# Optimization experiments

Hardware: AMD Instinct MI355X
Metric: run time of the kernel (lower is better)

Reference implementation:

```python
import jax, jax.numpy as jnp
import numpy as np

DEPTH = 12  # perfect binary tree: 2**DEPTH - 1 internal nodes, 2**DEPTH leaf children


def setup_inputs() -> dict:
    key = jax.random.key(0)
    k0, k1, k2, k3, k4 = jax.random.split(key, 5)
    H = 1024   # hidden_size
    I = 1024   # input_size
    N = 2 ** DEPTH - 1  # internal nodes, heap order (root = 0)
    scale = 0.02  # keep gates out of saturation
    emb = jax.random.normal(k0, (N, I), jnp.float32)
    W_ih = jax.random.normal(k1, (8 * H, I), jnp.float32) * scale
    W_hh = jax.random.normal(k2, (8 * H, 2 * H), jnp.float32) * scale
    b_ih = jax.random.normal(k3, (8 * H,), jnp.float32) * scale
    b_hh = jax.random.normal(k4, (8 * H,), jnp.float32) * scale
    return {"emb": emb, "W_ih": W_ih, "W_hh": W_hh, "b_ih": b_ih, "b_hh": b_hh}


def reference(emb, W_ih, W_hh, b_ih, b_hh):
    # Batched-by-level Tree-LSTM over a perfect binary tree in heap order.
    # nn.LSTM hidden size is 2H; node state passed upward is the first H dims.
    H2 = W_hh.shape[1]          # 2 * hidden_size
    H = H2 // 2
    b = b_ih + b_hh
    # Leaves: hidden = cell = zeros((1, H)) per the module's base case.
    h = jnp.zeros((2 ** DEPTH, H), emb.dtype)
    c = jnp.zeros((2 ** DEPTH, H), emb.dtype)
    for k in range(DEPTH - 1, -1, -1):  # bottom-up over levels
        n = 2 ** k
        # cat((a.hidden, b.hidden), dim=1): children of node j are 2j, 2j+1
        h_cat = h.reshape(n, H2)
        c_cat = c.reshape(n, H2)
        x = emb[n - 1: 2 * n - 1]  # level-k embeddings (heap indices n-1 .. 2n-2)
        gates = x @ W_ih.T + h_cat @ W_hh.T + b  # (n, 8H)
        i_, f_, g_, o_ = jnp.split(gates, 4, axis=1)  # PyTorch gate order i,f,g,o
        c_new = jax.nn.sigmoid(f_) * c_cat + jax.nn.sigmoid(i_) * jnp.tanh(g_)
        h_new = jax.nn.sigmoid(o_) * jnp.tanh(c_new)
        h = h_new[:, :H]  # slice back to hidden_size, as the module does
        c = c_new[:, :H]
    # root hidden and cell, each (1, H)
    return jnp.concatenate([h, c], axis=1)
```

## Files before the change

kernel.cpp:

```cpp
#include <hip/hip_runtime.h>
#include <hip/hip_bf16.h>
#include <math.h>


#define TREE_DEPTH 12

typedef unsigned short u16;
typedef unsigned int u32;
typedef __attribute__((ext_vector_type(8))) short bf16x8;
typedef __attribute__((ext_vector_type(4))) float f32x4;
typedef __attribute__((ext_vector_type(8))) unsigned short u16x8;
typedef __attribute__((ext_vector_type(2))) unsigned int u32x2;

__device__ __forceinline__ void gload16(const void* g, void* l) {
    __builtin_amdgcn_global_load_lds(
        (const __attribute__((address_space(1))) u32*)g,
        (__attribute__((address_space(3))) u32*)l, 16, 0, 0);
}

template <int N>
__device__ __forceinline__ void vmwait() {
    asm volatile("s_waitcnt vmcnt(%0)" :: "n"(N) : "memory");
}
__device__ __forceinline__ void rbar() {
    __builtin_amdgcn_sched_barrier(0);
    __builtin_amdgcn_s_barrier();
    __builtin_amdgcn_sched_barrier(0);
}

__device__ __forceinline__ u16 f2bf(float f) {
    __hip_bfloat16 h = __float2bfloat16(f);
    return *reinterpret_cast<u16*>(&h);
}
__device__ __forceinline__ u16 f2h(float f) {
    _Float16 h = (_Float16)f;
    return *reinterpret_cast<u16*>(&h);
}
__device__ __forceinline__ float h2f(u16 u) {
    _Float16 h;
    *reinterpret_cast<u16*>(&h) = u;
    return (float)h;
}
__device__ __forceinline__ float fsig(float x) {
    return 1.0f / (1.0f + __expf(-x));
}
__device__ __forceinline__ float ftanh(float x) {
    return 1.0f - 2.0f / (1.0f + __expf(2.0f * x));
}

__global__ void prep(const float* __restrict__ Wih,
                     const float* __restrict__ Whh,
                     const float* __restrict__ emb,
                     const float* __restrict__ b_ih,
                     const float* __restrict__ b_hh,
                     u16* __restrict__ Wih_p, u16* __restrict__ Whh_p,
                     u16* __restrict__ xb, float* __restrict__ bge) {
    const int bid = blockIdx.x;
    if (bid < 12288) {
        const int b = bid & 4095;
        const int seg = bid >> 12;
        const int x = b & 7, t = b >> 3;
        const int e = ((t & 3) * 8 + x) * 128 + (t >> 2);
        const int g = (e >> 4) & 3;
        const int j = (e >> 6) * 16 + (e & 15);
        const int wr = g * 2048 + j;
        const int col = threadIdx.x * 4;
        f32x4 v;
        u16* dst;
        if (seg == 0) {
            v = __builtin_nontemporal_load(
                (const f32x4*)(Wih + (size_t)wr * 1024 + col));
            dst = Wih_p + (size_t)e * 1024 + col;
        } else {
            v = __builtin_nontemporal_load(
                (const f32x4*)(Whh + (size_t)wr * 2048 + (seg - 1) * 1024 + col));
            dst = Whh_p + (size_t)e * 2048 + (seg - 1) * 1024 + col;
        }
        u32x2 p;
        p[0] = (u32)f2bf(v[0]) | ((u32)f2bf(v[1]) << 16);
        p[1] = (u32)f2bf(v[2]) | ((u32)f2bf(v[3]) << 16);
        *reinterpret_cast<u32x2*>(dst) = p;
    } else if (bid < 16383) {
        size_t idx = ((size_t)(bid - 12288) * 256 + threadIdx.x) * 4;
        f32x4 v = __builtin_nontemporal_load((const f32x4*)(emb + idx));
        u32x2 p;
        p[0] = (u32)f2bf(v[0]) | ((u32)f2bf(v[1]) << 16);
        p[1] = (u32)f2bf(v[2]) | ((u32)f2bf(v[3]) << 16);
        *reinterpret_cast<u32x2*>(xb + idx) = p;
    } else {
        int e = (bid - 16383) * 256 + threadIdx.x;
        int g = (e >> 4) & 3;
        int j = (e >> 6) * 16 + (e & 15);
        int r = g * 2048 + j;
        bge[e] = b_ih[r] + b_hh[r];
    }
}

__global__ __launch_bounds__(256) void gemm_gx(
    const u16* __restrict__ xb, const u16* __restrict__ Wp,
    const float* __restrict__ bge, u16* __restrict__ GX,
    u16* __restrict__ hdst, float* __restrict__ cdst)
{
    __shared__ u16 smem[32768];

    const int gx_ = gridDim.x;
    int b = blockIdx.x + gx_ * blockIdx.y;
    const int x = b & 7, t = b >> 3;
    const int ct = (t & 3) * 8 + x;
    const int mt = t >> 2;
    const int m0 = mt * 128, c0 = ct * 128;

    const int tid = threadIdx.x, lane = tid & 63, w = tid >> 6;
    const int wr = (w >> 1) * 64, wc = (w & 1) * 64;

    f32x4 acc[4][4];
    #pragma unroll
    for (int i = 0; i < 4; ++i)
        #pragma unroll
        for (int j = 0; j < 4; ++j)
            acc[i][j] = f32x4{0.f, 0.f, 0.f, 0.f};

    u16* bufs[2] = {smem, smem + 16384};
    const u16* gp[8];
    u16* dl0[8];
    u16* dl1[8];
    #pragma unroll
    for (int i = 0; i < 8; ++i) {
        const int s = tid + i * 256;
        const int r = s >> 3;
        const int o = (s & 7) * 16;
        const int ke = (o ^ ((r & 7) << 4)) >> 1;
        gp[i] = (r < 128) ? xb + (size_t)(m0 + r) * 1024 + ke
                          : Wp + (size_t)(c0 + r - 128) * 1024 + ke;
        dl0[i] = bufs[0] + s * 8;
        dl1[i] = bufs[1] + s * 8;
    }

    const int fl = lane & 15;
    const int kunit = (lane >> 4) * 16;

    #define STAGE0() { _Pragma("unroll") \
        for (int i = 0; i < 8; ++i) { gload16(gp[i], dl0[i]); gp[i] += 64; } }
    #define STAGE1() { _Pragma("unroll") \
        for (int i = 0; i < 8; ++i) { gload16(gp[i], dl1[i]); gp[i] += 64; } }

    #define COMPUTE(B) {                                                     \
        _Pragma("unroll")                                                    \
        for (int ks = 0; ks < 2; ++ks) {                                     \
            bf16x8 a_[4], b_[4];                                             \
            _Pragma("unroll")                                                \
            for (int i = 0; i < 4; ++i) {                                    \
                const int ar = wr + i * 16 + fl;                             \
                const int byo = (ks * 64 + kunit) ^ ((ar & 7) << 4);         \
                a_[i] = *reinterpret_cast<const bf16x8*>(                    \
                    reinterpret_cast<const char*>((B) + ar * 64) + byo);     \
            }                                                                \
            _Pragma("unroll")                                                \
            for (int j = 0; j < 4; ++j) {                                    \
                const int br = 128 + wc + j * 16 + fl;                       \
                const int byo = (ks * 64 + kunit) ^ ((br & 7) << 4);         \
                b_[j] = *reinterpret_cast<const bf16x8*>(                    \
                    reinterpret_cast<const char*>((B) + br * 64) + byo);     \
            }                                                                \
            _Pragma("unroll")                                                \
            for (int i = 0; i < 4; ++i)                                      \
                _Pragma("unroll")                                            \
                for (int j = 0; j < 4; ++j)                                  \
                    acc[i][j] = __builtin_amdgcn_mfma_f32_16x16x32_bf16(     \
                        a_[i], b_[j], acc[i][j], 0, 0, 0);                   \
        } }

    STAGE0();
    #pragma unroll 2
    for (int it = 0; it < 16; ++it) {
        const int cur = it & 1;
        if (it < 15) {
            if (cur == 0) STAGE1() else STAGE0();
            vmwait<8>();
        } else {
            vmwait<0>();
        }
        rbar();
        if (cur == 0) COMPUTE(bufs[0]) else COMPUTE(bufs[1]);
        rbar();
    }
    #undef STAGE0
    #undef STAGE1
    #undef COMPUTE

    const int rg = (lane >> 4) * 4;
    if (m0 < 2047) {
        #pragma unroll
        for (int i = 0; i < 4; ++i)
            #pragma unroll
            for (int j = 0; j < 4; ++j) {
                const float bv = bge[c0 + wc + j * 16 + fl];
                #pragma unroll
                for (int r = 0; r < 4; ++r)
                    smem[(wr + i * 16 + rg + r) * 140 + (wc + j * 16 + fl)] =
                        f2h(acc[i][j][r] + bv);
            }
        __syncthreads();
        const int row_ = tid >> 4, chunk = tid & 15;
        #pragma unroll
        for (int it = 0; it < 8; ++it) {
            const int row = it * 16 + row_;
            if (m0 + row < 2047) {
                u16x8 v = *reinterpret_cast<const u16x8*>(
                    &smem[row * 140 + chunk * 8]);
                __builtin_nontemporal_store(
                    v, (u16x8*)(GX + (size_t)(m0 + row) * 4096 + c0 + chunk * 8));
            }
        }
    }
    if (m0 + 127 >= 2047) {
        const int jj = ((c0 + wc) >> 6) * 16 + fl;
        const float bi  = bge[c0 + wc + fl];
        const float bgg = bge[c0 + wc + 32 + fl];
        const float bo  = bge[c0 + wc + 48 + fl];
        #pragma unroll
        for (int i = 0; i < 4; ++i) {
            #pragma unroll
            for (int r = 0; r < 4; ++r) {
                const int m = m0 + wr + i * 16 + rg + r;
                if (m < 2047 || m >= 4095) continue;
                const int mm = m - 2047;
                const float cn = fsig(acc[i][0][r] + bi) * ftanh(acc[i][2][r] + bgg);
                const float hn = fsig(acc[i][3][r] + bo) * ftanh(cn);
                hdst[(size_t)(mm >> 1) * 2048 + (mm & 1) * 1024 + jj] = f2bf(hn);
                if (!(mm & 1))
                    cdst[(size_t)(mm >> 1) * 1024 + jj] = cn;
            }
        }
    }
}

template <int MI, int MW, int NW, int KG>
__global__ __launch_bounds__(MW* NW* KG * 64) void fused_level(
    const u16* __restrict__ A, const u16* __restrict__ Wp,
    const u16* __restrict__ GXl, const float* __restrict__ cprev,
    u16* __restrict__ hnext, float* __restrict__ cnext,
    float* __restrict__ outp, int n)
{
    constexpr int BM = MI * 16 * MW;
    constexpr int BN = NW * 64;
    constexpr int S = MW * NW;
    constexpr int NFR = MI * 4;
    constexpr int RC = NFR > 8 ? 8 : NFR;
    constexpr int NP = NFR / RC;
    constexpr int ROWS = BM + BN;
    constexpr int SLOTS = ROWS * 8;
    constexpr int GT = S * 64;
    constexpr int NL = SLOTS / GT;
    static_assert(SLOTS % GT == 0, "slot mapping must be exact");
    constexpr int STG = KG * ROWS * 128;
    constexpr int REDB = (KG > 1) ? (KG - 1) * S * RC * 64 * 16 : 0;
    constexpr int SMEM = STG > REDB ? STG : REDB;
    __shared__ __align__(16) char smem[SMEM];

    const int gx_ = gridDim.x;
    int b = blockIdx.x + gx_ * blockIdx.y;
    const int x = b & 7;
    int t = b >> 3;
    int ct, mt;
    if constexpr (NW == 2) {
        ct = (t & 3) * 8 + x; mt = t >> 2;
    } else {
        const int lo = t & 1; t >>= 1;
        ct = ((t & 3) * 8 + x) * 2 + lo; mt = t >> 2;
    }
    const int m0 = mt * BM;
    const int c0 = ct * BN;

    const int tid = threadIdx.x;
    const int lane = tid & 63;
    const int w = tid >> 6;
    const int kg = w / S;
    const int slot = w % S;
    const int wm = slot / NW;
    const int wn = slot % NW;

    const int Kc = 2048 / KG;
    const int kbeg = kg * Kc;

    u16* buf = (u16*)smem + (size_t)kg * ROWS * 64;

    const int gtid = slot * 64 + lane;
    const u16* gp[NL];
    u16* dl[NL];
    #pragma unroll
    for (int i = 0; i < NL; ++i) {
        const int s = gtid + i * GT;
        const int r = s >> 3;
        const int o = (s & 7) * 16;
        const int ke = (o ^ ((r & 7) << 4)) >> 1;
        if (r < BM) {
            int ar = m0 + r;
            if (ar >= n) ar = n - 1;
            gp[i] = A + (size_t)ar * 2048 + kbeg + ke;
        } else {
            gp[i] = Wp + (size_t)(c0 + r - BM) * 2048 + kbeg + ke;
        }
        dl[i] = buf + s * 8;
    }

    f32x4 acc[MI][4];
    #pragma unroll
    for (int mi = 0; mi < MI; ++mi)
        #pragma unroll
        for (int f = 0; f < 4; ++f)
            acc[mi][f] = f32x4{0.f, 0.f, 0.f, 0.f};

    const int fl = lane & 15;
    const int kunit = (lane >> 4) * 16;
    const int ar0 = wm * MI * 16;
    const int bc0 = BM;

    for (int k0 = 0; k0 < Kc; k0 += 64) {
        #pragma unroll
        for (int i = 0; i < NL; ++i) { gload16(gp[i], dl[i]); gp[i] += 64; }
        __syncthreads();
        #pragma unroll
        for (int ks = 0; ks < 2; ++ks) {
            bf16x8 a_[MI], b_[4];
            #pragma unroll
            for (int mi = 0; mi < MI; ++mi) {
                const int ar = ar0 + mi * 16 + fl;
                const int byo = (ks * 64 + kunit) ^ ((ar & 7) << 4);
                a_[mi] = *reinterpret_cast<const bf16x8*>(
                    reinterpret_cast<const char*>(buf + ar * 64) + byo);
            }
            #pragma unroll
            for (int f = 0; f < 4; ++f) {
                const int br = bc0 + wn * 64 + f * 16 + fl;
                const int byo = (ks * 64 + kunit) ^ ((br & 7) << 4);
                b_[f] = *reinterpret_cast<const bf16x8*>(
                    reinterpret_cast<const char*>(buf + br * 64) + byo);
            }
            #pragma unroll
            for (int mi = 0; mi < MI; ++mi)
                #pragma unroll
                for (int f = 0; f < 4; ++f)
                    acc[mi][f] = __builtin_amdgcn_mfma_f32_16x16x32_bf16(
                        a_[mi], b_[f], acc[mi][f], 0, 0, 0);
        }
        __syncthreads();
    }

    if constexpr (KG > 1) {
        f32x4* red = reinterpret_cast<f32x4*>(smem);
        #pragma unroll
        for (int pass = 0; pass < NP; ++pass) {
            if (kg > 0) {
                #pragma unroll
                for (int f = 0; f < RC; ++f) {
                    const int fr = pass * RC + f;
                    red[(((kg - 1) * S + slot) * RC + f) * 64 + lane] =
                        acc[fr >> 2][fr & 3];
                }
            }
            __syncthreads();
            if (kg == 0) {
                #pragma unroll
                for (int q = 1; q < KG; ++q)
                    #pragma unroll
                    for (int f = 0; f < RC; ++f) {
                        const int fr = pass * RC + f;
                        f32x4 v = red[(((q - 1) * S + slot) * RC + f) * 64 + lane];
                        acc[fr >> 2][fr & 3][0] += v[0];
                        acc[fr >> 2][fr & 3][1] += v[1];
                        acc[fr >> 2][fr & 3][2] += v[2];
                        acc[fr >> 2][fr & 3][3] += v[3];
                    }
            }
            __syncthreads();
        }
    }

    if (kg != 0) return;
    const int j = ((c0 + wn * 64) >> 6) * 16 + fl;
    #pragma unroll
    for (int mi = 0; mi < MI; ++mi) {
        #pragma unroll
        for (int r = 0; r < 4; ++r) {
            const int m = m0 + wm * MI * 16 + mi * 16 + (lane >> 4) * 4 + r;
            if (m >= n) continue;
            const u16* gx = GXl + (size_t)m * 4096 + c0 + wn * 64 + fl;
            const float i_ = acc[mi][0][r] + h2f(__builtin_nontemporal_load(gx));
            const float f_ = acc[mi][1][r] + h2f(__builtin_nontemporal_load(gx + 16));
            const float g_ = acc[mi][2][r] + h2f(__builtin_nontemporal_load(gx + 32));
            const float o_ = acc[mi][3][r] + h2f(__builtin_nontemporal_load(gx + 48));
            const float cc = __builtin_nontemporal_load(cprev + (size_t)m * 1024 + j);
            const float cn = fsig(f_) * cc + fsig(i_) * ftanh(g_);
            const float hn = fsig(o_) * ftanh(cn);
            if (hnext)
                hnext[(size_t)(m >> 1) * 2048 + (m & 1) * 1024 + j] = f2bf(hn);
            if (!(m & 1))
                __builtin_nontemporal_store(cn, cnext + (size_t)(m >> 1) * 1024 + j);
            if (outp) { outp[j] = hn; outp[1024 + j] = cn; }
        }
    }
}

extern "C" void kernel_launch(void* const* d_in, const int* in_sizes, int n_in,
                              void* d_out, int out_size, void* d_ws, size_t ws_size,
                              hipStream_t stream) {
    const float* emb  = (const float*)d_in[0];
    const float* W_ih = (const float*)d_in[1];
    const float* W_hh = (const float*)d_in[2];
    const float* b_ih = (const float*)d_in[3];
    const float* b_hh = (const float*)d_in[4];
    float* out = (float*)d_out;

    char* p = (char*)d_ws;
    float* bge  = (float*)p;  p += 16384;
    u16* Wih_p  = (u16*)p;    p += (size_t)4096 * 1024 * 2;
    u16* Whh_p  = (u16*)p;    p += (size_t)4096 * 2048 * 2;
    u16* xb     = (u16*)p;    p += (size_t)4096 * 1024 * 2;
    u16* GX     = (u16*)p;    p += (size_t)4096 * 4096 * 2;
    u16* Hcat   = (u16*)p;    p += (size_t)4096 * 2048 * 2;
    float* cbA  = (float*)p;  p += (size_t)1024 * 1024 * 4;
    float* cbB  = (float*)p;  p += (size_t)1024 * 1024 * 4;

    prep<<<16399, 256, 0, stream>>>(W_ih, W_hh, emb, b_ih, b_hh,
                                    Wih_p, Whh_p, xb, bge);

    #define OFF(k) (4096 - (2 << (k)))

    gemm_gx<<<dim3(32, 32), 256, 0, stream>>>(
        xb, Wih_p, bge, GX, Hcat + (size_t)OFF(10) * 2048, cbA);

    const float* cprev = cbA;
    float* cbufs[2] = {cbB, cbA};
    int t = 0;
    for (int k = TREE_DEPTH - 2; k >= 0; --k) {
        const int n = 1 << k;
        const u16* A = Hcat + (size_t)OFF(k) * 2048;
        const u16* GXl = GX + (size_t)(n - 1) * 4096;
        u16* hnext = (k > 0) ? (Hcat + (size_t)OFF(k - 1) * 2048) : nullptr;
        float* cnext = cbufs[t];
        float* outp = (k == 0) ? out : nullptr;

        if (k == 10) {
            fused_level<4, 1, 2, 2><<<dim3(16, 32), 256, 0, stream>>>(
                A, Whh_p, GXl, cprev, hnext, cnext, outp, n);
        } else if (k == 9) {
            fused_level<2, 1, 2, 2><<<dim3(16, 32), 256, 0, stream>>>(
                A, Whh_p, GXl, cprev, hnext, cnext, outp, n);
        } else if (k == 8) {
            fused_level<1, 1, 1, 4><<<dim3(16, 64), 256, 0, stream>>>(
                A, Whh_p, GXl, cprev, hnext, cnext, outp, n);
        } else {
            const int gx = (n >= 16) ? n / 16 : 1;
            fused_level<1, 1, 1, 8><<<dim3(gx, 64), 512, 0, stream>>>(
                A, Whh_p, GXl, cprev, hnext, cnext, outp, n);
        }
        cprev = cnext; t ^= 1;
    }
}
```

Before: 222.3 us.

## Enlarge input-projection GEMM tiles to 256x256 with 8 waves per block

The gx GEMM moves from 128x128 tiles with 4 waves to 256x256 tiles with 8 waves, and each wave now computes a 128x64 sub-tile. Double-buffered shared memory grows to 128KB and the grid drops from 1024 to 256 blocks. The epilogue writes back through shared memory in two 128-row halves. Larger tiles raise arithmetic intensity and reduce redundant loads of W and x, at the cost of higher register pressure (32 accumulators), fewer blocks across the CUs, and one block per CU because of the shared-memory footprint.

```diff
diff --git a/kernel.cpp b/kernel.cpp
--- a/kernel.cpp
+++ b/kernel.cpp
@@ -96,42 +96,41 @@
     }
 }
 
-__global__ __launch_bounds__(256) void gemm_gx(
+__global__ __launch_bounds__(512) void gemm_gx(
     const u16* __restrict__ xb, const u16* __restrict__ Wp,
     const float* __restrict__ bge, u16* __restrict__ GX,
     u16* __restrict__ hdst, float* __restrict__ cdst)
 {
-    __shared__ u16 smem[32768];
-
-    const int gx_ = gridDim.x;
-    int b = blockIdx.x + gx_ * blockIdx.y;
+    __shared__ u16 smem[65536];
+
+    int b = blockIdx.x + 16 * blockIdx.y;
     const int x = b & 7, t = b >> 3;
-    const int ct = (t & 3) * 8 + x;
-    const int mt = t >> 2;
-    const int m0 = mt * 128, c0 = ct * 128;
+    const int ct = (t & 1) * 8 + x;
+    const int mt = t >> 1;
+    const int m0 = mt * 256, c0 = ct * 256;
 
     const int tid = threadIdx.x, lane = tid & 63, w = tid >> 6;
-    const int wr = (w >> 1) * 64, wc = (w & 1) * 64;
-
-    f32x4 acc[4][4];
+    const int wm = w >> 2, wn = w & 3;
+
+    f32x4 acc[8][4];
     #pragma unroll
-    for (int i = 0; i < 4; ++i)
+    for (int i = 0; i < 8; ++i)
         #pragma unroll
         for (int j = 0; j < 4; ++j)
             acc[i][j] = f32x4{0.f, 0.f, 0.f, 0.f};
 
-    u16* bufs[2] = {smem, smem + 16384};
+    u16* bufs[2] = {smem, smem + 32768};
     const u16* gp[8];
     u16* dl0[8];
     u16* dl1[8];
     #pragma unroll
     for (int i = 0; i < 8; ++i) {
-        const int s = tid + i * 256;
+        const int s = tid + i * 512;
         const int r = s >> 3;
         const int o = (s & 7) * 16;
         const int ke = (o ^ ((r & 7) << 4)) >> 1;
-        gp[i] = (r < 128) ? xb + (size_t)(m0 + r) * 1024 + ke
-                          : Wp + (size_t)(c0 + r - 128) * 1024 + ke;
+        gp[i] = (r < 256) ? xb + (size_t)(m0 + r) * 1024 + ke
+                          : Wp + (size_t)(c0 + r - 256) * 1024 + ke;
         dl0[i] = bufs[0] + s * 8;
         dl1[i] = bufs[1] + s * 8;
     }
@@ -144,30 +143,32 @@
     #define STAGE1() { _Pragma("unroll") \
         for (int i = 0; i < 8; ++i) { gload16(gp[i], dl1[i]); gp[i] += 64; } }
 
-    #define COMPUTE(B) {                                                     \
+    #define COMPUTE(BUF) {                                                   \
+        const u16* bA_ = (BUF);                                              \
+        const u16* bB_ = (BUF) + 16384;                                      \
         _Pragma("unroll")                                                    \
         for (int ks = 0; ks < 2; ++ks) {                                     \
-            bf16x8 a_[4], b_[4];                                             \
+            bf16x8 a_[8], b_[4];                                             \
             _Pragma("unroll")                                                \
-            for (int i = 0; i < 4; ++i) {                                    \
-                const int ar = wr + i * 16 + fl;                             \
+            for (int mi = 0; mi < 8; ++mi) {                                 \
+                const int ar = wm * 128 + mi * 16 + fl;                      \
                 const int byo = (ks * 64 + kunit) ^ ((ar & 7) << 4);         \
-                a_[i] = *reinterpret_cast<const bf16x8*>(                    \
-                    reinterpret_cast<const char*>((B) + ar * 64) + byo);     \
+                a_[mi] = *reinterpret_cast<const bf16x8*>(                   \
+                    reinterpret_cast<const char*>(bA_ + ar * 64) + byo);     \
             }                                                                \
             _Pragma("unroll")                                                \
-            for (int j = 0; j < 4; ++j) {                                    \
-                const int br = 128 + wc + j * 16 + fl;                       \
+            for (int f = 0; f < 4; ++f) {                                    \
+                const int br = wn * 64 + f * 16 + fl;                        \
                 const int byo = (ks * 64 + kunit) ^ ((br & 7) << 4);         \
-                b_[j] = *reinterpret_cast<const bf16x8*>(                    \
-                    reinterpret_cast<const char*>((B) + br * 64) + byo);     \
+                b_[f] = *reinterpret_cast<const bf16x8*>(                    \
+                    reinterpret_cast<const char*>(bB_ + br * 64) + byo);     \
             }                                                                \
             _Pragma("unroll")                                                \
-            for (int i = 0; i < 4; ++i)                                      \
+            for (int mi = 0; mi < 8; ++mi)                                   \
                 _Pragma("unroll")                                            \
-                for (int j = 0; j < 4; ++j)                                  \
-                    acc[i][j] = __builtin_amdgcn_mfma_f32_16x16x32_bf16(     \
-                        a_[i], b_[j], acc[i][j], 0, 0, 0);                   \
+                for (int f = 0; f < 4; ++f)                                  \
+                    acc[mi][f] = __builtin_amdgcn_mfma_f32_16x16x32_bf16(    \
+                        a_[mi], b_[f], acc[mi][f], 0, 0, 0);                 \
         } }
 
     STAGE0();
@@ -191,42 +192,50 @@
     const int rg = (lane >> 4) * 4;
     if (m0 < 2047) {
         #pragma unroll
-        for (int i = 0; i < 4; ++i)
-            #pragma unroll
-            for (int j = 0; j < 4; ++j) {
-                const float bv = bge[c0 + wc + j * 16 + fl];
+        for (int ch = 0; ch < 2; ++ch) {
+            __syncthreads();
+            if (wm == ch) {
                 #pragma unroll
-                for (int r = 0; r < 4; ++r)
-                    smem[(wr + i * 16 + rg + r) * 140 + (wc + j * 16 + fl)] =
-                        f2h(acc[i][j][r] + bv);
-            }
-        __syncthreads();
-        const int row_ = tid >> 4, chunk = tid & 15;
-        #pragma unroll
-        for (int it = 0; it < 8; ++it) {
-            const int row = it * 16 + row_;
-            if (m0 + row < 2047) {
-                u16x8 v = *reinterpret_cast<const u16x8*>(
-                    &smem[row * 140 + chunk * 8]);
-                __builtin_nontemporal_store(
-                    v, (u16x8*)(GX + (size_t)(m0 + row) * 4096 + c0 + chunk * 8));
-            }
-        }
-    }
-    if (m0 + 127 >= 2047) {
-        const int jj = ((c0 + wc) >> 6) * 16 + fl;
-        const float bi  = bge[c0 + wc + fl];
-        const float bgg = bge[c0 + wc + 32 + fl];
-        const float bo  = bge[c0 + wc + 48 + fl];
-        #pragma unroll
-        for (int i = 0; i < 4; ++i) {
+                for (int mi = 0; mi < 8; ++mi)
+                    #pragma unroll
+                    for (int f = 0; f < 4; ++f) {
+                        const int col = wn * 64 + f * 16 + fl;
+                        const float bv = bge[c0 + col];
+                        #pragma unroll
+                        for (int r = 0; r < 4; ++r)
+                            smem[(mi * 16 + rg + r) * 264 + col] =
+                                f2h(acc[mi][f][r] + bv);
+                    }
+            }
+            __syncthreads();
+            const int row = tid >> 2;
+            const int cb = (tid & 3) * 64;
+            const int gm = m0 + ch * 128 + row;
+            if (gm < 2047) {
+                #pragma unroll
+                for (int q = 0; q < 8; ++q) {
+                    u16x8 v = *reinterpret_cast<const u16x8*>(
+                        &smem[row * 264 + cb + q * 8]);
+                    __builtin_nontemporal_store(
+                        v, (u16x8*)(GX + (size_t)gm * 4096 + c0 + cb + q * 8));
+                }
+            }
+        }
+    }
+    if (m0 + 255 >= 2047) {
+        const int jj = ((c0 + wn * 64) >> 6) * 16 + fl;
+        const float bi  = bge[c0 + wn * 64 + fl];
+        const float bgg = bge[c0 + wn * 64 + 32 + fl];
+        const float bo  = bge[c0 + wn * 64 + 48 + fl];
+        #pragma unroll
+        for (int mi = 0; mi < 8; ++mi) {
             #pragma unroll
             for (int r = 0; r < 4; ++r) {
-                const int m = m0 + wr + i * 16 + rg + r;
+                const int m = m0 + wm * 128 + mi * 16 + rg + r;
                 if (m < 2047 || m >= 4095) continue;
                 const int mm = m - 2047;
-                const float cn = fsig(acc[i][0][r] + bi) * ftanh(acc[i][2][r] + bgg);
-                const float hn = fsig(acc[i][3][r] + bo) * ftanh(cn);
+                const float cn = fsig(acc[mi][0][r] + bi) * ftanh(acc[mi][2][r] + bgg);
+                const float hn = fsig(acc[mi][3][r] + bo) * ftanh(cn);
                 hdst[(size_t)(mm >> 1) * 2048 + (mm & 1) * 1024 + jj] = f2bf(hn);
                 if (!(mm & 1))
                     cdst[(size_t)(mm >> 1) * 1024 + jj] = cn;
@@ -427,7 +436,7 @@
 
     #define OFF(k) (4096 - (2 << (k)))
 
-    gemm_gx<<<dim3(32, 32), 256, 0, stream>>>(
+    gemm_gx<<<dim3(16, 16), 512, 0, stream>>>(
         xb, Wih_p, bge, GX, Hcat + (size_t)OFF(10) * 2048, cbA);
 
     const float* cprev = cbA;
```

Result: slower. 234.9 us (+5.7%).
